# Kernel optimization log

Hardware: AMD Instinct MI355X
Metric: run time of the kernel (lower is better)

Reference implementation:

```python
import jax, jax.numpy as jnp
import numpy as np

FRACTION = 0.33


def setup_inputs() -> dict:
    key = jax.random.key(0)
    kq, kk, kv = jax.random.split(key, 3)
    B, L_Q, L_K, D = 8, 4096, 4096, 512
    queries = jax.random.normal(kq, (B, L_Q, D), dtype=jnp.float32)
    keys = jax.random.normal(kk, (B, L_K, D), dtype=jnp.float32)
    values = jax.random.normal(kv, (B, L_K, D), dtype=jnp.float32)
    return {"queries": queries, "keys": keys, "values": values}


def reference(queries, keys, values):
    B, L_Q, D = queries.shape
    l_Q = int((1.0 - FRACTION) * L_Q)  # static: 2744

    # K_reduce: mean of per-feature top-l_Q key values (torch keys.topk(l_Q, dim=1))
    # top_k works on last axis -> transpose to [B, D, L_K]
    topk_vals = jax.lax.top_k(jnp.swapaxes(keys, 1, 2), l_Q)[0]  # [B, D, l_Q]
    K_reduce = jnp.mean(topk_vals, axis=-1)                       # [B, D]

    # score each query against reduced key, select top-l_Q queries
    sqk = jnp.einsum('bd,bqd->bq', K_reduce, queries)             # [B, L_Q]
    indices = jax.lax.top_k(sqk, l_Q)[1]                          # [B, l_Q] int32

    # gather selected queries
    Q_sample = jnp.take_along_axis(queries, indices[:, :, None], axis=1)  # [B, l_Q, D]

    # dense attention of selected queries over all keys
    QK = jnp.einsum('bqd,bkd->bqk', Q_sample, keys)               # [B, l_Q, L_K]
    scale = 1.0 / np.sqrt(D).astype(np.float32)
    attn = jax.nn.softmax(QK * scale, axis=-1)
    out_sel = jnp.einsum('bqk,bkd->bqd', attn, values)            # [B, l_Q, D]

    # non-selected queries get mean of values; scatter selected results back
    mean_values = jnp.mean(values, axis=-2)                       # [B, D]
    result = jnp.broadcast_to(mean_values[:, None, :], (B, L_Q, D))
    result = result.at[jnp.arange(B)[:, None], indices].set(out_sel)
    return result
```

## Files before the change

kernel.cpp:

```cpp
#include <hip/hip_runtime.h>
#include <math.h>

#define NB 8
#define LK 4096
#define LQ 4096
#define DD 512
#define LSEL 2744
#define LPAD 2816

typedef __attribute__((ext_vector_type(8))) short bf16x8;
typedef __attribute__((ext_vector_type(4))) float f32x4;
typedef __attribute__((ext_vector_type(16))) float f32x16;

#define AS1 __attribute__((address_space(1)))
#define AS3 __attribute__((address_space(3)))

__device__ __forceinline__ unsigned short f2bf(float x) {
  unsigned u = __float_as_uint(x);
  unsigned r = (u + 0x7fffu + ((u >> 16) & 1u)) >> 16;
  return (unsigned short)r;
}

__device__ __forceinline__ unsigned fkey(float x) {
  unsigned b = __float_as_uint(x);
  return (b & 0x80000000u) ? ~b : (b | 0x80000000u);
}

__device__ __forceinline__ unsigned cvt_pk_bf16(float lo, float hi) {
  unsigned r;
  asm("v_cvt_pk_bf16_f32 %0, %1, %2" : "=v"(r) : "v"(lo), "v"(hi));
  return r;
}

__global__ void k_transpose(const float* __restrict__ keys, float* __restrict__ keysT,
                            unsigned short* __restrict__ kbf) {
  __shared__ float tile[32][33];
  int b = blockIdx.z;
  int k0 = blockIdx.x * 32, d0 = blockIdx.y * 32;
  int tx = threadIdx.x, ty = threadIdx.y;
  const float* src = keys + ((size_t)b * LK + k0) * DD + d0;
#pragma unroll
  for (int i = 0; i < 4; i++) {
    float v = src[(size_t)(ty + 8 * i) * DD + tx];
    tile[ty + 8 * i][tx] = v;
    kbf[((size_t)b * LK + k0 + ty + 8 * i) * DD + d0 + tx] = f2bf(v);
  }
  __syncthreads();
  float* dst = keysT + ((size_t)b * DD + d0) * LK + k0;
#pragma unroll
  for (int i = 0; i < 4; i++) dst[(size_t)(ty + 8 * i) * LK + tx] = tile[tx][ty + 8 * i];
}

__global__ void k_vt(const float* __restrict__ values, unsigned short* __restrict__ vt,
                     float* __restrict__ part) {
  __shared__ float tile[32][65];
  __shared__ float psum[4][64];
  int b = blockIdx.z, k0 = blockIdx.x * 32, d0 = blockIdx.y * 64;
  int tid = threadIdx.x;
  const float* src = values + ((size_t)b * LK + k0) * DD + d0;
#pragma unroll
  for (int j = 0; j < 8; j++) {
    int li = tid + 256 * j;
    tile[li >> 6][li & 63] = src[(size_t)(li >> 6) * DD + (li & 63)];
  }
  __syncthreads();
  int c = tid >> 6, d = tid & 63;
  union { unsigned short us[8]; uint4 v; } pk;
  float fs = 0.f;
#pragma unroll
  for (int j = 0; j < 8; j++) {
    float v = tile[c * 8 + j][d];
    pk.us[j] = f2bf(v);
    fs += v;
  }
  size_t ci = ((size_t)b * (LK / 8) + (size_t)(k0 >> 3) + c) * DD + d0 + d;
  ((uint4*)vt)[ci] = pk.v;
  psum[c][d] = fs;
  __syncthreads();
  if (tid < 64) {
    float s = psum[0][tid] + psum[1][tid] + psum[2][tid] + psum[3][tid];
    part[((size_t)b * 128 + (k0 >> 5)) * DD + d0 + tid] = s;
  }
}

__global__ __launch_bounds__(256) void k_kreduce(const float* __restrict__ keysT, float* __restrict__ kred) {
  __shared__ unsigned keys[4096];
  __shared__ unsigned hist[256];
  __shared__ unsigned sh_pr[2];
  __shared__ double redd[256];
  __shared__ unsigned redu[256];
  int row = blockIdx.x;
  int tid = threadIdx.x;
  const float* src = keysT + (size_t)row * LK;
  for (int i = tid; i < LK; i += 256) keys[i] = fkey(src[i]);
  unsigned prefix = 0;
  int rank = LSEL;
  for (int shift = 24; shift >= 0; shift -= 8) {
    hist[tid] = 0;
    __syncthreads();
    for (int i = tid; i < LK; i += 256) {
      unsigned u = keys[i];
      if (((u >> shift) >> 8) == prefix) atomicAdd(&hist[(u >> shift) & 255], 1);
    }
    __syncthreads();
    if (tid == 0) {
      int r = rank;
      unsigned bin = 255;
      for (;;) {
        int c = (int)hist[bin];
        if (c >= r) break;
        r -= c;
        if (bin == 0) break;
        bin--;
      }
      sh_pr[0] = (prefix << 8) | bin;
      sh_pr[1] = (unsigned)r;
    }
    __syncthreads();
    prefix = sh_pr[0];
    rank = (int)sh_pr[1];
  }
  double fsum = 0.0;
  unsigned fcnt = 0;
  for (int i = tid; i < LK; i += 256) {
    unsigned u = keys[i];
    if (u > prefix) {
      unsigned bits = (u & 0x80000000u) ? (u ^ 0x80000000u) : ~u;
      fsum += (double)__uint_as_float(bits);
      fcnt++;
    }
  }
  redd[tid] = fsum; redu[tid] = fcnt;
  __syncthreads();
  for (int s = 128; s > 0; s >>= 1) {
    if (tid < s) { redd[tid] += redd[tid + s]; redu[tid] += redu[tid + s]; }
    __syncthreads();
  }
  if (tid == 0) {
    unsigned u = prefix;
    unsigned bits = (u & 0x80000000u) ? (u ^ 0x80000000u) : ~u;
    float tval = __uint_as_float(bits);
    kred[row] = (float)((redd[0] + (double)(LSEL - (int)redu[0]) * (double)tval) / (double)LSEL);
  }
}

__global__ __launch_bounds__(256) void k_sqk(const float* __restrict__ queries, const float* __restrict__ kred,
                                             float* __restrict__ sqk) {
  int gw = blockIdx.x * 4 + (threadIdx.x >> 6);
  int lane = threadIdx.x & 63;
  int b = gw >> 12;
  const float* qp = queries + (size_t)gw * DD;
  const float* kp = kred + (size_t)b * DD;
  float4 a0 = ((const float4*)qp)[lane * 2];
  float4 a1 = ((const float4*)qp)[lane * 2 + 1];
  float4 c0 = ((const float4*)kp)[lane * 2];
  float4 c1 = ((const float4*)kp)[lane * 2 + 1];
  double s = (double)a0.x * c0.x + (double)a0.y * c0.y + (double)a0.z * c0.z + (double)a0.w * c0.w +
             (double)a1.x * c1.x + (double)a1.y * c1.y + (double)a1.z * c1.z + (double)a1.w * c1.w;
#pragma unroll
  for (int m = 1; m < 64; m <<= 1) s += __shfl_xor(s, m);
  if (lane == 0) sqk[gw] = (float)s;
}

__global__ __launch_bounds__(512) void k_select(const float* __restrict__ sqk, int* __restrict__ qidx,
                                                unsigned char* __restrict__ selflag) {
  __shared__ float vals[4096];
  __shared__ unsigned hist[16];
  __shared__ unsigned wsum[8];
  int b = blockIdx.x, tid = threadIdx.x;
  const float* src = sqk + (size_t)b * LQ;
  for (int i = tid; i < LQ; i += 512) vals[i] = src[i];
  __syncthreads();
  unsigned prefix = 0;
  int rank = LSEL;
  for (int shift = 28; shift >= 0; shift -= 4) {
    if (tid < 16) hist[tid] = 0;
    __syncthreads();
    unsigned cnt[16];
#pragma unroll
    for (int j = 0; j < 16; j++) cnt[j] = 0;
    for (int i = tid; i < LQ; i += 512) {
      unsigned u = fkey(vals[i]);
      if (((u >> shift) >> 4) == prefix) cnt[(u >> shift) & 15]++;
    }
#pragma unroll
    for (int j = 0; j < 16; j++) if (cnt[j]) atomicAdd(&hist[j], cnt[j]);
    __syncthreads();
    int r = rank;
    unsigned bin = 15;
    for (;;) {
      int c = (int)hist[bin];
      if (c >= r) break;
      r -= c;
      if (bin == 0) break;
      bin--;
    }
    prefix = (prefix << 4) | bin;
    rank = r;
    __syncthreads();
  }
  unsigned gt = 0, eq = 0;
#pragma unroll
  for (int j = 0; j < 8; j++) {
    int i = tid * 8 + j;
    unsigned u = fkey(vals[i]);
    gt += (u > prefix) ? 1u : 0u;
    eq += (u == prefix) ? 1u : 0u;
  }
  unsigned packed = (gt << 16) | eq;
  unsigned x = packed;
  int lane = tid & 63, wv = tid >> 6;
#pragma unroll
  for (int off2 = 1; off2 < 64; off2 <<= 1) {
    unsigned t = __shfl_up(x, off2);
    if (lane >= off2) x += t;
  }
  if (lane == 63) wsum[wv] = x;
  __syncthreads();
  unsigned wpre = 0, total = 0;
#pragma unroll
  for (int i = 0; i < 8; i++) {
    unsigned v = wsum[i];
    if (i < wv) wpre += v;
    total += v;
  }
  unsigned exclv = x + wpre - packed;
  unsigned total_gt = total >> 16;
  unsigned need_eq = (unsigned)LSEL - total_gt;
  unsigned gpos = exclv >> 16;
  unsigned epos = exclv & 0xffffu;
  for (int j = 0; j < 8; j++) {
    int i = tid * 8 + j;
    unsigned u = fkey(vals[i]);
    unsigned char fl = 0;
    if (u > prefix) {
      qidx[(size_t)b * LPAD + gpos] = i;
      gpos++;
      fl = 1;
    } else if (u == prefix) {
      if (epos < need_eq) {
        qidx[(size_t)b * LPAD + total_gt + epos] = i;
        fl = 1;
      }
      epos++;
    }
    selflag[(size_t)b * LQ + i] = fl;
  }
  for (int p = LSEL + tid; p < LPAD; p += 512) qidx[(size_t)b * LPAD + p] = -1;
}

__global__ void k_gather(const float* __restrict__ queries, const int* __restrict__ qidx,
                         unsigned short* __restrict__ qs) {
  const float QSCL = 0.04419417418f * 1.4426950408889634f;
  int r = blockIdx.x, b = blockIdx.y;
  int tid = threadIdx.x;
  int q = qidx[(size_t)b * LPAD + r];
  ushort4* dst = (ushort4*)(qs + ((size_t)b * LPAD + r) * DD);
  if (q < 0) {
    ushort4 z; z.x = 0; z.y = 0; z.z = 0; z.w = 0;
    dst[tid] = z;
  } else {
    const float4* srcv = (const float4*)(queries + ((size_t)b * LQ + q) * DD);
    float4 v = srcv[tid];
    ushort4 o;
    o.x = f2bf(v.x * QSCL); o.y = f2bf(v.y * QSCL);
    o.z = f2bf(v.z * QSCL); o.w = f2bf(v.w * QSCL);
    dst[tid] = o;
  }
}

__global__ void k_meanv_fin(const float* __restrict__ part, float* __restrict__ meanv) {
  int d = blockIdx.x * 256 + threadIdx.x;
  int b = blockIdx.y;
  float s = 0.f;
  for (int i = 0; i < 128; i++) s += part[((size_t)b * 128 + i) * DD + d];
  meanv[(size_t)b * DD + d] = s * (1.0f / 4096.0f);
}

__global__ void k_fill(float4* __restrict__ out4, const float4* __restrict__ mv4,
                       const unsigned char* __restrict__ flag) {
  int row = blockIdx.x * 2 + (threadIdx.x >> 7);
  int t = threadIdx.x & 127;
  if (flag[row]) return;
  int b = row >> 12;
  out4[(size_t)row * 128 + t] = mv4[b * 128 + t];
}

__global__ __launch_bounds__(512, 2) void k_attn(const unsigned short* __restrict__ qs,
                                                 const unsigned short* __restrict__ kbf,
                                                 const unsigned short* __restrict__ vt,
                                                 const int* __restrict__ qidx,
                                                 float* __restrict__ out) {
  extern __shared__ char smem[];
  int bi = blockIdx.x;
  int b = bi & 7;
  int q0 = (bi >> 3) * 128;
  int tid = threadIdx.x;
  int w = tid >> 6, lane = tid & 63;
  int l31 = lane & 31, h = lane >> 5;
  int qg = w >> 1, dg = w & 1;

  const unsigned short* qrow = qs + ((size_t)b * LPAD + q0 + qg * 32 + l31) * DD + dg * 256;
  bf16x8 qb[16];
#pragma unroll
  for (int t = 0; t < 16; t++) qb[t] = *(const bf16x8*)(qrow + t * 16 + h * 8);

  f32x16 O[8];
#pragma unroll
  for (int n = 0; n < 8; n++)
#pragma unroll
    for (int j = 0; j < 16; j++) O[n][j] = 0.f;
  float m_run = -1e30f, l_run = 0.f;

  const char* gK = (const char*)(kbf + (size_t)b * LK * DD);
  const char* gV = (const char*)vt;

#define STAGE(KT, BUF)                                                                          \
  do {                                                                                          \
    char* Kd = smem + (size_t)(BUF)*65536;                                                      \
    char* Vd = Kd + 32768;                                                                      \
    const char* ksrc = gK + (size_t)(KT)*32768 + (size_t)l31 * 1024 + h * 16;                   \
    const char* vsrc = gV + ((size_t)b * 512 + (size_t)(KT)*4) * 8192 + lane * 16;              \
    _Pragma("unroll") for (int j = 0; j < 4; j++) {                                             \
      int u = w + 8 * j;                                                                        \
      __builtin_amdgcn_global_load_lds((const AS1 unsigned int*)(uintptr_t)(ksrc + u * 32),     \
                                       (AS3 unsigned int*)(uintptr_t)(Kd + u * 1024 +           \
                                                                      lane * 16),               \
                                       16, 0, 0);                                               \
    }                                                                                           \
    _Pragma("unroll") for (int j = 0; j < 4; j++) {                                             \
      int s = w + 8 * j;                                                                        \
      __builtin_amdgcn_global_load_lds((const AS1 unsigned int*)(uintptr_t)(vsrc + s * 1024),   \
                                       (AS3 unsigned int*)(uintptr_t)(Vd + s * 1024 +           \
                                                                      lane * 16),               \
                                       16, 0, 0);                                               \
    }                                                                                           \
  } while (0)

  STAGE(0, 0);
  __syncthreads();
  int cur = 0;

  char* mySx = smem + 131072 + (size_t)w * 4096;
  const char* pSx = smem + 131072 + (size_t)(w ^ 1) * 4096;

  for (int kt = 0; kt < LK / 32; kt++) {
    if (kt + 1 < LK / 32) STAGE(kt + 1, cur ^ 1);

    const char* Kl = smem + (size_t)cur * 65536;
    const char* Vl = Kl + 32768;

    f32x16 acc;
#pragma unroll
    for (int j = 0; j < 16; j++) acc[j] = 0.f;
    const char* Kp = Kl + (size_t)(dg * 32 + h) * 512 + l31 * 16;
    __builtin_amdgcn_s_setprio(1);
#pragma unroll
    for (int t = 0; t < 16; t++) {
      bf16x8 kf = *(const bf16x8*)(Kp + t * 1024);
      acc = __builtin_amdgcn_mfma_f32_32x32x16_bf16(kf, qb[t], acc, 0, 0, 0);
    }
    __builtin_amdgcn_s_setprio(0);

#pragma unroll
    for (int j = 0; j < 4; j++) {
      f32x4 v4 = {acc[4 * j], acc[4 * j + 1], acc[4 * j + 2], acc[4 * j + 3]};
      *(f32x4*)(mySx + j * 1024 + lane * 16) = v4;
    }
    asm volatile("s_waitcnt lgkmcnt(0)\ns_barrier" ::: "memory");
#pragma unroll
    for (int j = 0; j < 4; j++) {
      f32x4 v4 = *(const f32x4*)(pSx + j * 1024 + lane * 16);
      acc[4 * j] += v4[0];
      acc[4 * j + 1] += v4[1];
      acc[4 * j + 2] += v4[2];
      acc[4 * j + 3] += v4[3];
    }

    float mx = acc[0];
#pragma unroll
    for (int r = 1; r < 16; r++) mx = fmaxf(mx, acc[r]);
    mx = fmaxf(mx, __shfl_xor(mx, 32));
    if (!__all(mx - m_run <= 11.5f)) {
      float mn = fmaxf(m_run, mx);
      float f = exp2f(m_run - mn);
      m_run = mn;
      l_run *= f;
#pragma unroll
      for (int r = 0; r < 16; r++) {
        float fr = __shfl(f, (r & 3) + 8 * (r >> 2) + 4 * h);
#pragma unroll
        for (int n = 0; n < 8; n++) O[n][r] *= fr;
      }
    }
    float ps = 0.f;
#pragma unroll
    for (int r = 0; r < 16; r++) {
      acc[r] = exp2f(acc[r] - m_run);
      ps += acc[r];
    }
    l_run += ps;

    unsigned pw[8], px[8];
#pragma unroll
    for (int i = 0; i < 8; i++) pw[i] = cvt_pk_bf16(acc[2 * i], acc[2 * i + 1]);
#pragma unroll
    for (int i = 0; i < 8; i++) px[i] = __shfl_xor(pw[i], 32);
    union { unsigned u[4]; bf16x8 v; } A0, A1;
    A0.u[0] = h ? px[2] : pw[0];
    A0.u[1] = h ? px[3] : pw[1];
    A0.u[2] = h ? pw[2] : px[0];
    A0.u[3] = h ? pw[3] : px[1];
    A1.u[0] = h ? px[6] : pw[4];
    A1.u[1] = h ? px[7] : pw[5];
    A1.u[2] = h ? pw[6] : px[4];
    A1.u[3] = h ? pw[7] : px[5];

    const char* Vp = Vl + (size_t)h * 8192 + dg * 4096 + l31 * 16;
    __builtin_amdgcn_s_setprio(1);
#pragma unroll
    for (int n = 0; n < 8; n++) {
      bf16x8 b0 = *(const bf16x8*)(Vp + n * 512);
      O[n] = __builtin_amdgcn_mfma_f32_32x32x16_bf16(A0.v, b0, O[n], 0, 0, 0);
      bf16x8 b1 = *(const bf16x8*)(Vp + 16384 + n * 512);
      O[n] = __builtin_amdgcn_mfma_f32_32x32x16_bf16(A1.v, b1, O[n], 0, 0, 0);
    }
    __builtin_amdgcn_s_setprio(0);

    __syncthreads();
    cur ^= 1;
  }

  float lt = l_run + __shfl_xor(l_run, 32);
  float linv = 1.0f / lt;
  const int* qx = qidx + (size_t)b * LPAD + q0 + qg * 32;
#pragma unroll
  for (int r = 0; r < 16; r++) {
    int row = (r & 3) + 8 * (r >> 2) + 4 * h;
    float sc = __shfl(linv, row);
    int qq = qx[row];
    if (qq >= 0) {
      float* orow = out + ((size_t)b * LQ + qq) * DD + dg * 256 + l31;
#pragma unroll
      for (int n = 0; n < 8; n++) orow[n * 32] = O[n][r] * sc;
    }
  }
#undef STAGE
}

extern "C" void kernel_launch(void* const* d_in, const int* in_sizes, int n_in,
                              void* d_out, int out_size, void* d_ws, size_t ws_size,
                              hipStream_t stream) {
  const float* queries = (const float*)d_in[0];
  const float* keys = (const float*)d_in[1];
  const float* values = (const float*)d_in[2];
  float* out = (float*)d_out;
  char* ws = (char*)d_ws;
  size_t off = 0;
  float* keysT = (float*)(ws + off); off += (size_t)NB * DD * LK * 4;
  unsigned short* kbf = (unsigned short*)(ws + off); off += (size_t)NB * LK * DD * 2;
  unsigned short* vt = (unsigned short*)(ws + off); off += (size_t)NB * LK * DD * 2;
  float* kred = (float*)(ws + off); off += (size_t)NB * DD * 4;
  float* sqkv = (float*)(ws + off); off += (size_t)NB * LQ * 4;
  int* qidx = (int*)(ws + off); off += (size_t)NB * LPAD * 4;
  float* part = (float*)(ws + off); off += (size_t)NB * 128 * DD * 4;
  float* meanv = (float*)(ws + off); off += (size_t)NB * DD * 4;
  unsigned char* selflag = (unsigned char*)(ws + off); off += (size_t)NB * LQ;
  unsigned short* qs = (unsigned short*)keysT;

  hipFuncSetAttribute((const void*)k_attn, hipFuncAttributeMaxDynamicSharedMemorySize, 163840);

  k_transpose<<<dim3(LK / 32, DD / 32, NB), dim3(32, 8), 0, stream>>>(keys, keysT, kbf);
  k_vt<<<dim3(LK / 32, DD / 64, NB), 256, 0, stream>>>(values, vt, part);
  k_kreduce<<<NB * DD, 256, 0, stream>>>(keysT, kred);
  k_sqk<<<NB * LQ / 4, 256, 0, stream>>>(queries, kred, sqkv);
  k_select<<<NB, 512, 0, stream>>>(sqkv, qidx, selflag);
  k_gather<<<dim3(LPAD, NB), 128, 0, stream>>>(queries, qidx, qs);
  k_meanv_fin<<<dim3(DD / 256, NB), 256, 0, stream>>>(part, meanv);
  k_fill<<<NB * LQ / 2, 256, 0, stream>>>((float4*)out, (const float4*)meanv, selflag);
  k_attn<<<dim3((LPAD / 128) * NB), 512, 163840, stream>>>(qs, kbf, vt, qidx, out);
}
```

Measured before the change: 676.0 us.

## Load K fragments directly from global memory and add two-level radix bin search

Result: slower. 966.3 us (+42.9%).

```diff
diff --git a/kernel.cpp b/kernel.cpp
--- a/kernel.cpp
+++ b/kernel.cpp
@@ -86,6 +86,7 @@
 __global__ __launch_bounds__(256) void k_kreduce(const float* __restrict__ keysT, float* __restrict__ kred) {
   __shared__ unsigned keys[4096];
   __shared__ unsigned hist[256];
+  __shared__ unsigned sup[16];
   __shared__ unsigned sh_pr[2];
   __shared__ double redd[256];
   __shared__ unsigned redu[256];
@@ -103,17 +104,32 @@
       if (((u >> shift) >> 8) == prefix) atomicAdd(&hist[(u >> shift) & 255], 1);
     }
     __syncthreads();
+    if (tid < 16) {
+      unsigned s = 0;
+#pragma unroll
+      for (int j = 0; j < 16; j++) s += hist[tid * 16 + j];
+      sup[tid] = s;
+    }
+    __syncthreads();
     if (tid == 0) {
       int r = rank;
-      unsigned bin = 255;
+      int sb = 15;
+      for (;;) {
+        int c = (int)sup[sb];
+        if (c >= r) break;
+        r -= c;
+        if (sb == 0) break;
+        sb--;
+      }
+      int bin = sb * 16 + 15;
       for (;;) {
         int c = (int)hist[bin];
         if (c >= r) break;
         r -= c;
-        if (bin == 0) break;
+        if (bin == sb * 16) break;
         bin--;
       }
-      sh_pr[0] = (prefix << 8) | bin;
+      sh_pr[0] = (prefix << 8) | (unsigned)bin;
       sh_pr[1] = (unsigned)r;
     }
     __syncthreads();
@@ -317,17 +333,8 @@
 
 #define STAGE(KT, BUF)                                                                          \
   do {                                                                                          \
-    char* Kd = smem + (size_t)(BUF)*65536;                                                      \
-    char* Vd = Kd + 32768;                                                                      \
-    const char* ksrc = gK + (size_t)(KT)*32768 + (size_t)l31 * 1024 + h * 16;                   \
+    char* Vd = smem + (size_t)(BUF)*32768;                                                      \
     const char* vsrc = gV + ((size_t)b * 512 + (size_t)(KT)*4) * 8192 + lane * 16;              \
-    _Pragma("unroll") for (int j = 0; j < 4; j++) {                                             \
-      int u = w + 8 * j;                                                                        \
-      __builtin_amdgcn_global_load_lds((const AS1 unsigned int*)(uintptr_t)(ksrc + u * 32),     \
-                                       (AS3 unsigned int*)(uintptr_t)(Kd + u * 1024 +           \
-                                                                      lane * 16),               \
-                                       16, 0, 0);                                               \
-    }                                                                                           \
     _Pragma("unroll") for (int j = 0; j < 4; j++) {                                             \
       int s = w + 8 * j;                                                                        \
       __builtin_amdgcn_global_load_lds((const AS1 unsigned int*)(uintptr_t)(vsrc + s * 1024),   \
@@ -341,25 +348,37 @@
   __syncthreads();
   int cur = 0;
 
-  char* mySx = smem + 131072 + (size_t)w * 4096;
-  const char* pSx = smem + 131072 + (size_t)(w ^ 1) * 4096;
+  char* mySx = smem + 65536 + (size_t)w * 4096;
+  const char* pSx = smem + 65536 + (size_t)(w ^ 1) * 4096;
 
   for (int kt = 0; kt < LK / 32; kt++) {
     if (kt + 1 < LK / 32) STAGE(kt + 1, cur ^ 1);
 
-    const char* Kl = smem + (size_t)cur * 65536;
-    const char* Vl = Kl + 32768;
+    const char* Vl = smem + (size_t)cur * 32768;
+
+    const char* kp = gK + (size_t)kt * 32768 + (size_t)l31 * 1024 + dg * 512 + h * 16;
+    bf16x8 kf0[4], kf1[4];
+#pragma unroll
+    for (int j = 0; j < 4; j++) kf0[j] = *(const bf16x8*)(kp + j * 32);
+#pragma unroll
+    for (int j = 0; j < 4; j++) kf1[j] = *(const bf16x8*)(kp + (4 + j) * 32);
 
     f32x16 acc;
 #pragma unroll
     for (int j = 0; j < 16; j++) acc[j] = 0.f;
-    const char* Kp = Kl + (size_t)(dg * 32 + h) * 512 + l31 * 16;
     __builtin_amdgcn_s_setprio(1);
 #pragma unroll
-    for (int t = 0; t < 16; t++) {
-      bf16x8 kf = *(const bf16x8*)(Kp + t * 1024);
-      acc = __builtin_amdgcn_mfma_f32_32x32x16_bf16(kf, qb[t], acc, 0, 0, 0);
-    }
+    for (int j = 0; j < 4; j++) acc = __builtin_amdgcn_mfma_f32_32x32x16_bf16(kf0[j], qb[j], acc, 0, 0, 0);
+#pragma unroll
+    for (int j = 0; j < 4; j++) kf0[j] = *(const bf16x8*)(kp + (8 + j) * 32);
+#pragma unroll
+    for (int j = 0; j < 4; j++) acc = __builtin_amdgcn_mfma_f32_32x32x16_bf16(kf1[j], qb[4 + j], acc, 0, 0, 0);
+#pragma unroll
+    for (int j = 0; j < 4; j++) kf1[j] = *(const bf16x8*)(kp + (12 + j) * 32);
+#pragma unroll
+    for (int j = 0; j < 4; j++) acc = __builtin_amdgcn_mfma_f32_32x32x16_bf16(kf0[j], qb[8 + j], acc, 0, 0, 0);
+#pragma unroll
+    for (int j = 0; j < 4; j++) acc = __builtin_amdgcn_mfma_f32_32x32x16_bf16(kf1[j], qb[12 + j], acc, 0, 0, 0);
     __builtin_amdgcn_s_setprio(0);
 
 #pragma unroll
@@ -468,7 +487,7 @@
   unsigned char* selflag = (unsigned char*)(ws + off); off += (size_t)NB * LQ;
   unsigned short* qs = (unsigned short*)keysT;
 
-  hipFuncSetAttribute((const void*)k_attn, hipFuncAttributeMaxDynamicSharedMemorySize, 163840);
+  hipFuncSetAttribute((const void*)k_attn, hipFuncAttributeMaxDynamicSharedMemorySize, 98304);
 
   k_transpose<<<dim3(LK / 32, DD / 32, NB), dim3(32, 8), 0, stream>>>(keys, keysT, kbf);
   k_vt<<<dim3(LK / 32, DD / 64, NB), 256, 0, stream>>>(values, vt, part);
@@ -478,5 +497,5 @@
   k_gather<<<dim3(LPAD, NB), 128, 0, stream>>>(queries, qidx, qs);
   k_meanv_fin<<<dim3(DD / 256, NB), 256, 0, stream>>>(part, meanv);
   k_fill<<<NB * LQ / 2, 256, 0, stream>>>((float4*)out, (const float4*)meanv, selflag);
-  k_attn<<<dim3((LPAD / 128) * NB), 512, 163840, stream>>>(qs, kbf, vt, qidx, out);
-}
+  k_attn<<<dim3((LPAD / 128) * NB), 512, 98304, stream>>>(qs, kbf, vt, qidx, out);
+}
```
